# Optimization experiments

Measured on AMD Instinct MI355X. Metric: run time of the kernel, lower is better.

Reference implementation:

```python
import jax, jax.numpy as jnp
import numpy as np

N_NODES = 50000
N_EDGES = 800000
IN_DIM = 128
HID = 32
HEADS = 3
OUT_DIM = 128
NEG_SLOPE = 0.2  # PyG GATConv default leaky_relu slope
EPS = 1e-16


def setup_inputs() -> dict:
    key = jax.random.key(0)
    ks = jax.random.split(key, 16)
    x = jax.random.normal(ks[0], (N_NODES, IN_DIM), jnp.float32)
    edge_index = jax.random.randint(ks[1], (2, N_EDGES), 0, N_NODES, dtype=jnp.int32)
    s = 0.1
    return {
        'x': x,
        'edge_index': edge_index,
        # layer 1: in=128 -> heads=3, c=32, concat
        'W1': jax.random.normal(ks[2], (IN_DIM, HEADS * HID), jnp.float32) * s,
        'as1': jax.random.normal(ks[3], (HEADS, HID), jnp.float32) * s,
        'ad1': jax.random.normal(ks[4], (HEADS, HID), jnp.float32) * s,
        'b1': jnp.zeros((HEADS * HID,), jnp.float32),
        # layer 2: in=96 -> heads=3, c=32, concat
        'W2': jax.random.normal(ks[5], (HEADS * HID, HEADS * HID), jnp.float32) * s,
        'as2': jax.random.normal(ks[6], (HEADS, HID), jnp.float32) * s,
        'ad2': jax.random.normal(ks[7], (HEADS, HID), jnp.float32) * s,
        'b2': jnp.zeros((HEADS * HID,), jnp.float32),
        # layer 3: in=96 -> heads=1, c=128, mean (concat=False)
        'W3': jax.random.normal(ks[8], (HEADS * HID, OUT_DIM), jnp.float32) * s,
        'as3': jax.random.normal(ks[9], (1, OUT_DIM), jnp.float32) * s,
        'ad3': jax.random.normal(ks[10], (1, OUT_DIM), jnp.float32) * s,
        'b3': jnp.zeros((OUT_DIM,), jnp.float32),
    }


def _gat_layer(x, src, dst, W, a_s, a_d, b, concat):
    # x: [N, F_in]; src/dst: [E'] (self-loops already appended)
    n = x.shape[0]
    heads, c = a_s.shape
    h = (x @ W).reshape(n, heads, c)                      # [N, H, C]
    alpha_src = jnp.sum(h * a_s[None], axis=-1)           # [N, H]
    alpha_dst = jnp.sum(h * a_d[None], axis=-1)           # [N, H]
    e = jax.nn.leaky_relu(alpha_src[src] + alpha_dst[dst], NEG_SLOPE)  # [E', H]
    # segment softmax over incoming edges of each dst node
    m = jax.ops.segment_max(e, dst, num_segments=n)       # [N, H] (every node has a self-loop)
    e = jnp.exp(e - m[dst])
    denom = jax.ops.segment_sum(e, dst, num_segments=n)   # [N, H]
    alpha = e / (denom[dst] + EPS)                        # [E', H]
    # attention dropout: module is evaluated in inference mode -> identity
    out = jax.ops.segment_sum(alpha[:, :, None] * h[src], dst, num_segments=n)  # [N, H, C]
    out = out.reshape(n, heads * c) if concat else out.mean(axis=1)
    return out + b


def reference(x, edge_index, W1, as1, ad1, b1, W2, as2, ad2, b2, W3, as3, ad3, b3):
    n = x.shape[0]
    loops = jnp.arange(n, dtype=edge_index.dtype)
    src = jnp.concatenate([edge_index[0], loops])  # PyG add_self_loops=True
    dst = jnp.concatenate([edge_index[1], loops])
    h = _gat_layer(x, src, dst, W1, as1, ad1, b1, concat=True)
    h = jax.nn.elu(h)
    h = _gat_layer(h, src, dst, W2, as2, ad2, b2, concat=True)
    h = jax.nn.elu(h)
    out = _gat_layer(h, src, dst, W3, as3, ad3, b3, concat=False)
    return out
```

## Files before the change

kernel.cpp:

```cpp
#include <hip/hip_runtime.h>
#include <hip/hip_bf16.h>
#include <hip/hip_fp16.h>
#include <math.h>

#define N_NODES_C 50000
#define NEG_SLOPE 0.2f
#define EPS_ 1e-16f

typedef _Float16 f16x8 __attribute__((ext_vector_type(8)));
typedef float    f32x4 __attribute__((ext_vector_type(4)));

__device__ __forceinline__ float lrelu(float x){ return x > 0.f ? x : NEG_SLOPE * x; }

__global__ void hist_k(const int* __restrict__ dstv, int* __restrict__ counts, int E){
  int t = blockIdx.x * blockDim.x + threadIdx.x;
  if (t < E) atomicAdd(&counts[dstv[t]], 1);
}

__global__ void chunksum_k(const int* __restrict__ counts, int* __restrict__ sums, int n){
  __shared__ int lds[4];
  int base = blockIdx.x * 1024;
  int t = threadIdx.x;
  int s = 0;
  for (int i = t; i < 1024; i += 256){ int idx = base + i; s += (idx < n) ? counts[idx] : 0; }
  for (int d = 32; d >= 1; d >>= 1) s += __shfl_xor(s, d);
  if ((t & 63) == 0) lds[t >> 6] = s;
  __syncthreads();
  if (t == 0) sums[blockIdx.x] = lds[0] + lds[1] + lds[2] + lds[3];
}

__global__ void chunkscan_k(const int* __restrict__ sums, int* __restrict__ offs,
                            int* __restrict__ row_ptr, int nblocks, int n){
  int l = threadIdx.x;
  int v = (l < nblocks) ? sums[l] : 0;
  int x = v;
  for (int d = 1; d < 64; d <<= 1){ int y = __shfl_up(x, d); if (l >= d) x += y; }
  if (l < nblocks) offs[l] = x - v;
  if (l == nblocks - 1) row_ptr[n] = x;
}

__global__ void scan_k(const int* __restrict__ counts, const int* __restrict__ offs,
                       int* __restrict__ row_ptr, int* __restrict__ fill, int n){
  __shared__ int ws[16];
  int base = blockIdx.x * 1024; int t = threadIdx.x; int idx = base + t;
  int v = (idx < n) ? counts[idx] : 0;
  int lane = t & 63, wid = t >> 6;
  int x = v;
  for (int d = 1; d < 64; d <<= 1){ int y = __shfl_up(x, d); if (lane >= d) x += y; }
  if (lane == 63) ws[wid] = x;
  __syncthreads();
  if (t < 16){ int y = ws[t]; for (int d = 1; d < 16; d <<= 1){ int z = __shfl_up(y, d); if (t >= d) y += z; } ws[t] = y; }
  __syncthreads();
  int excl = x - v + (wid ? ws[wid - 1] : 0) + offs[blockIdx.x];
  if (idx < n){ row_ptr[idx] = excl; fill[idx] = excl; }
}

__global__ void scatter_k(const int* __restrict__ srcv, const int* __restrict__ dstv,
                          int* __restrict__ fill, int* __restrict__ esrc, int E){
  int t = blockIdx.x * blockDim.x + threadIdx.x;
  if (t < E){ int p = atomicAdd(&fill[dstv[t]], 1); esrc[p] = srcv[t]; }
}

template<int K, int J>
__global__ void wpack_k(const float* __restrict__ W, uint4* __restrict__ Wf){
  constexpr int KS = K / 32, NT = J / 16;
  int tot = KS * NT * 64;
  for (int t = blockIdx.x * blockDim.x + threadIdx.x; t < tot; t += gridDim.x * blockDim.x){
    int l = t & 63;
    int nt = (t >> 6) % NT;
    int kk = t / (64 * NT);
    int col = nt * 16 + (l & 15);
    int k0 = kk * 32 + (l >> 4) * 8;
    unsigned u[4];
    #pragma unroll
    for (int p = 0; p < 4; p++){
      __half2 h = __floats2half2_rn(W[(k0 + 2 * p) * J + col], W[(k0 + 2 * p + 1) * J + col]);
      u[p] = *reinterpret_cast<unsigned*>(&h);
    }
    uint4 v; v.x = u[0]; v.y = u[1]; v.z = u[2]; v.w = u[3];
    Wf[t] = v;
  }
}

template<int K, int J, int HEADS, bool AF16>
__global__ __launch_bounds__(256) void gemm_mfma_k(
    const void* __restrict__ Ain, const uint4* __restrict__ Wf,
    const float* __restrict__ a_s, const float* __restrict__ a_d,
    __half* __restrict__ Hh, float* __restrict__ asrc, float* __restrict__ adst, int n){
  constexpr int KS = K / 32;
  constexpr int NT = J / 16;
  constexpr int CPR = K / 8;
  constexpr int NTPH = NT / HEADS;
  __shared__ uint4 Alds[64 * 16];
  int t = threadIdx.x;
  int rbase = blockIdx.x * 64;

  for (int i = t; i < 64 * CPR; i += 256){
    int r = i / CPR, c = i % CPR;
    int gr = rbase + r;
    uint4 v = make_uint4(0u, 0u, 0u, 0u);
    if (gr < n){
      if (AF16){
        v = ((const uint4*)Ain)[(size_t)gr * CPR + c];
      } else {
        const float4* af = (const float4*)Ain + (size_t)gr * (K / 4) + c * 2;
        float4 lo = af[0], hi = af[1];
        __half2 p0 = __floats2half2_rn(lo.x, lo.y);
        __half2 p1 = __floats2half2_rn(lo.z, lo.w);
        __half2 p2 = __floats2half2_rn(hi.x, hi.y);
        __half2 p3 = __floats2half2_rn(hi.z, hi.w);
        v.x = *reinterpret_cast<unsigned*>(&p0);
        v.y = *reinterpret_cast<unsigned*>(&p1);
        v.z = *reinterpret_cast<unsigned*>(&p2);
        v.w = *reinterpret_cast<unsigned*>(&p3);
      }
    }
    Alds[r * 16 + (c ^ (r & 7))] = v;
  }
  __syncthreads();

  int l = t & 63;
  int wrow = (t >> 6) * 16;
  int sub = l & 15;
  int lk = l >> 4;
  f32x4 acc[NT];
  #pragma unroll
  for (int i = 0; i < NT; i++) acc[i] = (f32x4){0.f, 0.f, 0.f, 0.f};

  for (int kk = 0; kk < KS; kk++){
    int trow = wrow + sub;
    int c = kk * 4 + lk;
    f16x8 a = *reinterpret_cast<const f16x8*>(&Alds[trow * 16 + (c ^ (trow & 7))]);
    const uint4* wb = Wf + (size_t)(kk * NT) * 64 + l;
    #pragma unroll
    for (int nt = 0; nt < NT; nt++){
      uint4 wv = wb[nt * 64];
      f16x8 b = *reinterpret_cast<const f16x8*>(&wv);
      acc[nt] = __builtin_amdgcn_mfma_f32_16x16x32_f16(a, b, acc[nt], 0, 0, 0);
    }
  }

  float ps[HEADS][4], pd[HEADS][4];
  #pragma unroll
  for (int h = 0; h < HEADS; h++)
    #pragma unroll
    for (int r = 0; r < 4; r++){ ps[h][r] = 0.f; pd[h][r] = 0.f; }
  #pragma unroll
  for (int nt = 0; nt < NT; nt++){
    int h = nt / NTPH;
    float sa = a_s[nt * 16 + sub];
    float sd = a_d[nt * 16 + sub];
    #pragma unroll
    for (int r = 0; r < 4; r++){ ps[h][r] += acc[nt][r] * sa; pd[h][r] += acc[nt][r] * sd; }
  }
  #pragma unroll
  for (int h = 0; h < HEADS; h++)
    #pragma unroll
    for (int r = 0; r < 4; r++)
      #pragma unroll
      for (int d = 1; d < 16; d <<= 1){
        ps[h][r] += __shfl_xor(ps[h][r], d);
        pd[h][r] += __shfl_xor(pd[h][r], d);
      }

  #pragma unroll
  for (int r = 0; r < 4; r++){
    int gr = rbase + wrow + lk * 4 + r;
    if (gr < n){
      #pragma unroll
      for (int nt = 0; nt < NT; nt++)
        Hh[(size_t)gr * J + nt * 16 + sub] = __float2half(acc[nt][r]);
    }
  }
  #pragma unroll
  for (int h = 0; h < HEADS; h++){
    if (sub == h){
      #pragma unroll
      for (int r = 0; r < 4; r++){
        int gr = rbase + wrow + lk * 4 + r;
        if (gr < n){
          asrc[gr * HEADS + h] = ps[h][r];
          adst[gr * HEADS + h] = pd[h][r];
        }
      }
    }
  }
}

template<int HEADS, int C, bool ELU, bool OUT16>
__global__ void agg_k(const __half* __restrict__ Hh,
                      const float* __restrict__ asrc, const float* __restrict__ adst,
                      const int* __restrict__ row_ptr, const int* __restrict__ esrc,
                      const float* __restrict__ bias, void* __restrict__ outv, int n){
  constexpr int J = HEADS * C;
  constexpr int NL = J / 2;
  int node = blockIdx.x * (blockDim.x >> 6) + (threadIdx.x >> 6);
  if (node >= n) return;
  int lane = threadIdx.x & 63;
  if (lane >= NL) return;
  int c0 = 2 * lane;
  int hh = c0 / C;
  const __half2* hp = (const __half2*)Hh;

  float ad = adst[node * HEADS + hh];
  float wself = __expf(lrelu(asrc[node * HEADS + hh] + ad));
  float2 hs = __half22float2(hp[(size_t)node * NL + lane]);
  float acc0 = wself * hs.x, acc1 = wself * hs.y, den = wself;

  int beg = row_ptr[node], end = row_ptr[node + 1];
  int e = beg;
  for (; e + 4 <= end; e += 4){
    int s[4]; float w[4]; float2 h[4];
    #pragma unroll
    for (int u = 0; u < 4; u++) s[u] = esrc[e + u];
    #pragma unroll
    for (int u = 0; u < 4; u++) w[u] = __expf(lrelu(asrc[s[u] * HEADS + hh] + ad));
    #pragma unroll
    for (int u = 0; u < 4; u++) h[u] = __half22float2(hp[(size_t)s[u] * NL + lane]);
    #pragma unroll
    for (int u = 0; u < 4; u++){ acc0 += w[u] * h[u].x; acc1 += w[u] * h[u].y; den += w[u]; }
  }
  for (; e < end; e++){
    int s = esrc[e];
    float w = __expf(lrelu(asrc[s * HEADS + hh] + ad));
    float2 h = __half22float2(hp[(size_t)s * NL + lane]);
    acc0 += w * h.x; acc1 += w * h.y; den += w;
  }
  float inv = 1.f / (den + EPS_);
  float r0 = acc0 * inv + bias[c0];
  float r1 = acc1 * inv + bias[c0 + 1];
  if (ELU){
    r0 = r0 > 0.f ? r0 : __expf(r0) - 1.f;
    r1 = r1 > 0.f ? r1 : __expf(r1) - 1.f;
  }
  if (OUT16){
    ((__half2*)outv)[(size_t)node * NL + lane] = __floats2half2_rn(r0, r1);
  } else {
    *reinterpret_cast<float2*>((float*)outv + (size_t)node * J + c0) = make_float2(r0, r1);
  }
}

extern "C" void kernel_launch(void* const* d_in, const int* in_sizes, int n_in,
                              void* d_out, int out_size, void* d_ws, size_t ws_size,
                              hipStream_t stream){
  const float* x   = (const float*)d_in[0];
  const int*   ei  = (const int*)  d_in[1];
  const float* W1  = (const float*)d_in[2];
  const float* as1 = (const float*)d_in[3];
  const float* ad1 = (const float*)d_in[4];
  const float* b1  = (const float*)d_in[5];
  const float* W2  = (const float*)d_in[6];
  const float* as2 = (const float*)d_in[7];
  const float* ad2 = (const float*)d_in[8];
  const float* b2  = (const float*)d_in[9];
  const float* W3  = (const float*)d_in[10];
  const float* as3 = (const float*)d_in[11];
  const float* ad3 = (const float*)d_in[12];
  const float* b3  = (const float*)d_in[13];
  float* out = (float*)d_out;

  const int N = N_NODES_C;
  const int E = in_sizes[1] / 2;
  const int* srcv = ei;
  const int* dstv = ei + E;

  char* ws = (char*)d_ws;
  auto alloc = [&](size_t bytes)->char*{ char* p = ws; ws += (bytes + 255) & ~(size_t)255; return p; };
  int*    counts  = (int*)   alloc((size_t)N * 4);
  int*    row_ptr = (int*)   alloc((size_t)(N + 1) * 4);
  int*    fill    = (int*)   alloc((size_t)N * 4);
  int*    csums   = (int*)   alloc(64 * 4);
  int*    coffs   = (int*)   alloc(64 * 4);
  int*    esrc    = (int*)   alloc((size_t)E * 4);
  __half* Hh      = (__half*)alloc((size_t)N * 128 * 2);
  __half* feat_h  = (__half*)alloc((size_t)N * 96 * 2);
  float*  a_src   = (float*) alloc((size_t)N * 3 * 4);
  float*  a_dst   = (float*) alloc((size_t)N * 3 * 4);
  uint4*  Wf1     = (uint4*) alloc(128 * 96 * 2);
  uint4*  Wf2     = (uint4*) alloc(96 * 96 * 2);
  uint4*  Wf3     = (uint4*) alloc(96 * 128 * 2);

  hipMemsetAsync(counts, 0, (size_t)N * 4, stream);
  hist_k<<<(E + 255) / 256, 256, 0, stream>>>(dstv, counts, E);
  int nch = (N + 1023) / 1024;
  chunksum_k<<<nch, 256, 0, stream>>>(counts, csums, N);
  chunkscan_k<<<1, 64, 0, stream>>>(csums, coffs, row_ptr, nch, N);
  scan_k<<<nch, 1024, 0, stream>>>(counts, coffs, row_ptr, fill, N);
  scatter_k<<<(E + 255) / 256, 256, 0, stream>>>(srcv, dstv, fill, esrc, E);

  wpack_k<128, 96><<<6, 256, 0, stream>>>(W1, Wf1);
  wpack_k<96, 96><<<5, 256, 0, stream>>>(W2, Wf2);
  wpack_k<96, 128><<<6, 256, 0, stream>>>(W3, Wf3);

  int gnode4 = (N + 3) / 4;
  int ggemm  = (N + 63) / 64;

  gemm_mfma_k<128, 96, 3, false><<<ggemm, 256, 0, stream>>>(x, Wf1, as1, ad1, Hh, a_src, a_dst, N);
  agg_k<3, 32, true, true><<<gnode4, 256, 0, stream>>>(Hh, a_src, a_dst, row_ptr, esrc, b1, feat_h, N);

  gemm_mfma_k<96, 96, 3, true><<<ggemm, 256, 0, stream>>>(feat_h, Wf2, as2, ad2, Hh, a_src, a_dst, N);
  agg_k<3, 32, true, true><<<gnode4, 256, 0, stream>>>(Hh, a_src, a_dst, row_ptr, esrc, b2, feat_h, N);

  gemm_mfma_k<96, 128, 1, true><<<ggemm, 256, 0, stream>>>(feat_h, Wf3, as3, ad3, Hh, a_src, a_dst, N);
  agg_k<1, 128, false, false><<<gnode4, 256, 0, stream>>>(Hh, a_src, a_dst, row_ptr, esrc, b3, out, N);
}
```

Baseline: 361.3 us.

## Replace atomic CSR scatter with two-pass LDS bucket sort by destination

```diff
diff --git a/kernel.cpp b/kernel.cpp
--- a/kernel.cpp
+++ b/kernel.cpp
@@ -4,6 +4,7 @@
 #include <math.h>
 
 #define N_NODES_C 50000
+#define NBKT ((N_NODES_C + 255) / 256)
 #define NEG_SLOPE 0.2f
 #define EPS_ 1e-16f
 
@@ -55,10 +56,58 @@
   if (idx < n){ row_ptr[idx] = excl; fill[idx] = excl; }
 }
 
-__global__ void scatter_k(const int* __restrict__ srcv, const int* __restrict__ dstv,
-                          int* __restrict__ fill, int* __restrict__ esrc, int E){
-  int t = blockIdx.x * blockDim.x + threadIdx.x;
-  if (t < E){ int p = atomicAdd(&fill[dstv[t]], 1); esrc[p] = srcv[t]; }
+__global__ void binit_k(const int* __restrict__ row_ptr, int* __restrict__ bcur){
+  int b = blockIdx.x * blockDim.x + threadIdx.x;
+  if (b < NBKT) bcur[b] = row_ptr[b * 256];
+}
+
+#define BATCH 2048
+#define BCAP 32
+__global__ __launch_bounds__(256) void bucket_k(const int* __restrict__ srcv, const int* __restrict__ dstv,
+                                                int* __restrict__ bcur, unsigned* __restrict__ ebuf, int E){
+  __shared__ unsigned stage[NBKT * BCAP];
+  __shared__ int cnt[NBKT];
+  int t = threadIdx.x;
+  int start = blockIdx.x * BATCH;
+  int end = start + BATCH; if (end > E) end = E;
+  for (int i = t; i < NBKT; i += 256) cnt[i] = 0;
+  __syncthreads();
+  for (int e = start + t; e < end; e += 256){
+    int s = srcv[e], d = dstv[e];
+    int b = d >> 8;
+    unsigned entry = (unsigned)s | ((unsigned)(d & 255) << 16);
+    int pos = atomicAdd(&cnt[b], 1);
+    if (pos < BCAP) stage[b * BCAP + pos] = entry;
+    else { int p = atomicAdd(&bcur[b], 1); ebuf[p] = entry; }
+  }
+  __syncthreads();
+  if (t < NBKT){
+    int c = cnt[t]; if (c > BCAP) c = BCAP;
+    if (c > 0){
+      int p = atomicAdd(&bcur[t], c);
+      for (int i = 0; i < c; i++) ebuf[p + i] = stage[t * BCAP + i];
+    }
+  }
+}
+
+__global__ __launch_bounds__(256) void bsort_k(const unsigned* __restrict__ ebuf,
+                                               const int* __restrict__ row_ptr,
+                                               int* __restrict__ esrc, int n){
+  __shared__ int cnt[256];
+  int b = blockIdx.x;
+  int nb = b * 256;
+  int t = threadIdx.x;
+  cnt[t] = 0;
+  __syncthreads();
+  int hi_node = nb + 256; if (hi_node > n) hi_node = n;
+  int beg = row_ptr[nb], end = row_ptr[hi_node];
+  for (int i = beg + t; i < end; i += 256){
+    unsigned e = ebuf[i];
+    int dl = e >> 16;
+    int src = (int)(e & 0xFFFFu);
+    int rank = atomicAdd(&cnt[dl], 1);
+    esrc[row_ptr[nb + dl] + rank] = src;
+  }
 }
 
 template<int K, int J>
@@ -135,8 +184,8 @@
     #pragma unroll
     for (int nt = 0; nt < NT; nt++){
       uint4 wv = wb[nt * 64];
-      f16x8 b = *reinterpret_cast<const f16x8*>(&wv);
-      acc[nt] = __builtin_amdgcn_mfma_f32_16x16x32_f16(a, b, acc[nt], 0, 0, 0);
+      f16x8 bfr = *reinterpret_cast<const f16x8*>(&wv);
+      acc[nt] = __builtin_amdgcn_mfma_f32_16x16x32_f16(a, bfr, acc[nt], 0, 0, 0);
     }
   }
 
@@ -266,19 +315,21 @@
 
   char* ws = (char*)d_ws;
   auto alloc = [&](size_t bytes)->char*{ char* p = ws; ws += (bytes + 255) & ~(size_t)255; return p; };
-  int*    counts  = (int*)   alloc((size_t)N * 4);
-  int*    row_ptr = (int*)   alloc((size_t)(N + 1) * 4);
-  int*    fill    = (int*)   alloc((size_t)N * 4);
-  int*    csums   = (int*)   alloc(64 * 4);
-  int*    coffs   = (int*)   alloc(64 * 4);
-  int*    esrc    = (int*)   alloc((size_t)E * 4);
-  __half* Hh      = (__half*)alloc((size_t)N * 128 * 2);
-  __half* feat_h  = (__half*)alloc((size_t)N * 96 * 2);
-  float*  a_src   = (float*) alloc((size_t)N * 3 * 4);
-  float*  a_dst   = (float*) alloc((size_t)N * 3 * 4);
-  uint4*  Wf1     = (uint4*) alloc(128 * 96 * 2);
-  uint4*  Wf2     = (uint4*) alloc(96 * 96 * 2);
-  uint4*  Wf3     = (uint4*) alloc(96 * 128 * 2);
+  int*      counts  = (int*)     alloc((size_t)N * 4);
+  int*      row_ptr = (int*)     alloc((size_t)(N + 1) * 4);
+  int*      fill    = (int*)     alloc((size_t)N * 4);
+  int*      csums   = (int*)     alloc(64 * 4);
+  int*      coffs   = (int*)     alloc(64 * 4);
+  int*      bcur    = (int*)     alloc(NBKT * 4);
+  int*      esrc    = (int*)     alloc((size_t)E * 4);
+  unsigned* ebuf    = (unsigned*)alloc((size_t)E * 4);
+  __half*   Hh      = (__half*)  alloc((size_t)N * 128 * 2);
+  __half*   feat_h  = (__half*)  alloc((size_t)N * 96 * 2);
+  float*    a_src   = (float*)   alloc((size_t)N * 3 * 4);
+  float*    a_dst   = (float*)   alloc((size_t)N * 3 * 4);
+  uint4*    Wf1     = (uint4*)   alloc(128 * 96 * 2);
+  uint4*    Wf2     = (uint4*)   alloc(96 * 96 * 2);
+  uint4*    Wf3     = (uint4*)   alloc(96 * 128 * 2);
 
   hipMemsetAsync(counts, 0, (size_t)N * 4, stream);
   hist_k<<<(E + 255) / 256, 256, 0, stream>>>(dstv, counts, E);
@@ -286,7 +337,9 @@
   chunksum_k<<<nch, 256, 0, stream>>>(counts, csums, N);
   chunkscan_k<<<1, 64, 0, stream>>>(csums, coffs, row_ptr, nch, N);
   scan_k<<<nch, 1024, 0, stream>>>(counts, coffs, row_ptr, fill, N);
-  scatter_k<<<(E + 255) / 256, 256, 0, stream>>>(srcv, dstv, fill, esrc, E);
+  binit_k<<<1, 256, 0, stream>>>(row_ptr, bcur);
+  bucket_k<<<(E + BATCH - 1) / BATCH, 256, 0, stream>>>(srcv, dstv, bcur, ebuf, E);
+  bsort_k<<<NBKT, 256, 0, stream>>>(ebuf, row_ptr, esrc, N);
 
   wpack_k<128, 96><<<6, 256, 0, stream>>>(W1, Wf1);
   wpack_k<96, 96><<<5, 256, 0, stream>>>(W2, Wf2);
```

New measurement: 335.3 us. -7.2%, faster.
